# Kernel optimization log

Measured on AMD Instinct MI355X. Metric: run time of the kernel, lower is better.

Reference implementation:

```python
import jax, jax.numpy as jnp
import numpy as np

B, TMAX, C, H, NCLS = 256, 512, 128, 256, 400


def _lengths():
    rs = np.random.RandomState(0)
    lens = rs.randint(128, TMAX + 1, size=B)
    lens[0] = TMAX  # pin max length so T = TMAX
    return lens


def setup_inputs() -> dict:
    lens = _lengths()
    total = int(lens.sum())
    key = jax.random.key(0)
    ks = jax.random.split(key, 12)
    s_in, s_h = 1.0 / np.sqrt(C), 1.0 / np.sqrt(H)
    return {
        "input_features": jax.random.normal(ks[0], (total, C), jnp.float32),
        "segment_lengths": jnp.asarray(lens, jnp.int32),
        "W_ih": jax.random.normal(ks[1], (4 * H, C), jnp.float32) * s_h,
        "W_hh": jax.random.normal(ks[2], (4 * H, H), jnp.float32) * s_h,
        "b_ih": jax.random.normal(ks[3], (4 * H,), jnp.float32) * s_h,
        "b_hh": jax.random.normal(ks[4], (4 * H,), jnp.float32) * s_h,
        "h0_W1": jax.random.normal(ks[5], (C, C), jnp.float32) * s_in,
        "h0_W2": jax.random.normal(ks[6], (H, C), jnp.float32) * s_in,
        "c0_W1": jax.random.normal(ks[7], (C, C), jnp.float32) * s_in,
        "c0_W2": jax.random.normal(ks[8], (H, C), jnp.float32) * s_in,
        "fc_W": jax.random.normal(ks[9], (NCLS, H), jnp.float32) * s_h,
        "fc_b": jax.random.normal(ks[10], (NCLS,), jnp.float32) * s_h,
    }


def _lstm_step(x, h, c, W_ih, W_hh, b_ih, b_hh):
    # torch.nn.LSTMCell gate order: i, f, g, o
    gates = x @ W_ih.T + b_ih + h @ W_hh.T + b_hh
    i, f, g, o = jnp.split(gates, 4, axis=-1)
    c_new = jax.nn.sigmoid(f) * c + jax.nn.sigmoid(i) * jnp.tanh(g)
    h_new = jax.nn.sigmoid(o) * jnp.tanh(c_new)
    return h_new, c_new


def reference(input_features, segment_lengths, W_ih, W_hh, b_ih, b_hh,
              h0_W1, h0_W2, c0_W1, c0_W2, fc_W, fc_b):
    lens = np.asarray(segment_lengths)            # static ragged structure
    nb = lens.shape[0]
    T = int(lens.max())
    seg_id = np.repeat(np.arange(nb), lens)       # [total]
    offs = np.concatenate([np.arange(l) for l in lens])
    dt = input_features.dtype

    # pad_sequence(batch_first=True): [B, T, C]
    padded = jnp.zeros((nb, T, input_features.shape[1]), dt)
    padded = padded.at[jnp.asarray(seg_id), jnp.asarray(offs)].set(input_features)

    # 'input_means' in the original is actually a per-segment SUM
    sums = jax.ops.segment_sum(input_features, jnp.asarray(seg_id), num_segments=nb)
    h0 = jax.nn.relu(sums @ h0_W1.T) @ h0_W2.T
    c0 = jax.nn.relu(sums @ c0_W1.T) @ c0_W2.T

    def step(carry, x_t):
        h, c = carry
        h, c = _lstm_step(x_t, h, c, W_ih, W_hh, b_ih, b_hh)
        return (h, c), h

    xs = jnp.transpose(padded, (1, 0, 2))         # [T, B, C]
    _, h_outs = jax.lax.scan(step, (h0, c0), xs)  # [T, B, H]

    # Faithful to the original: h_outs is stacked time-first, yet indexed
    # h_outs[i, :segment_len] with i = batch index -> for segment i, mean over
    # the first min(len_i, B) BATCH rows of the hidden state at time t=i.
    lens_j = jnp.asarray(lens)
    mask = (jnp.arange(nb)[None, :] < lens_j[:, None]).astype(dt)   # [B(i), B(b)]
    count = jnp.minimum(lens_j, nb).astype(dt)                       # slice clamps at B
    fc_in = jnp.einsum('ib,ibh->ih', mask, h_outs[:nb]) / count[:, None]

    return fc_in @ fc_W.T + fc_b
```

## Files before the change

### kernel.cpp

```cpp
#include <hip/hip_runtime.h>
#include <hip/hip_bf16.h>
#include <stdint.h>

#define NB    256
#define CIN   128
#define HID   256
#define TST   256
#define NCLS  400

#define GRPS  16
#define MEMB  4
#define BPG   16
#define HPB   64
#define RPB   256
#define HXS   392
#define SPP   17

#define WS_SUMS   0u
#define WS_HEX0   131072u
#define WS_HEX    262144u
#define WS_C0     524288u
#define WS_PP     786432u

typedef __attribute__((ext_vector_type(8))) short bf16x8;
typedef __attribute__((ext_vector_type(4))) float f32x4;
typedef unsigned long long u64;

__device__ __forceinline__ short f2bf(float f) {
  __hip_bfloat16 h = __float2bfloat16(f);
  return *reinterpret_cast<short*>(&h);
}
__device__ __forceinline__ float sigm(float v) { return 1.0f / (1.0f + __expf(-v)); }
__device__ __forceinline__ float tanh_(float v) {
  v = fminf(fmaxf(v, -15.0f), 15.0f);
  const float e = __expf(2.0f * v);
  return (e - 1.0f) / (e + 1.0f);
}
__device__ __forceinline__ int q12(float h) {
  int q = (int)rintf(h * 2048.f);
  q = max(-2048, min(2047, q));
  return q & 0xFFF;
}
__device__ __forceinline__ short dq12(int bits) {
  int q = (bits ^ 0x800) - 0x800;
  return f2bf((float)q * (1.0f / 2048.f));
}

__global__ void k_segsum(const float* __restrict__ x, const int* __restrict__ lens,
                         float* __restrict__ sums) {
  const int b = blockIdx.x, t = threadIdx.x;
  __shared__ int   s_l[NB];
  __shared__ int   s_red[256];
  __shared__ float s_f[CIN];
  s_l[t] = lens[t];
  __syncthreads();
  int part = 0;
  for (int i = t; i < b; i += 256) part += s_l[i];
  s_red[t] = part; __syncthreads();
  for (int k = 128; k > 0; k >>= 1) { if (t < k) s_red[t] += s_red[t + k]; __syncthreads(); }
  const int off = s_red[0];
  const int len = s_l[b];
  const int c = t & 127, half = t >> 7;
  float a = 0.f;
  for (int r = half; r < len; r += 2) a += x[(size_t)(off + r) * CIN + c];
  if (half) s_f[c] = a;
  __syncthreads();
  if (!half) sums[b * CIN + c] = a + s_f[c];
}

__global__ void k_init(const float* __restrict__ sums,
                       const float* __restrict__ w1h, const float* __restrict__ w2h,
                       const float* __restrict__ w1c, const float* __restrict__ w2c,
                       u64* __restrict__ hex0, float* __restrict__ c0) {
  const int b = blockIdx.x, t = threadIdx.x;
  __shared__ float s_in[CIN], s_h[CIN], s_c[CIN];
  __shared__ __align__(8) short s_hb[HID];
  if (t < CIN) s_in[t] = sums[b * CIN + t];
  __syncthreads();
  {
    const int j = t & 127;
    const float* w = (t < CIN ? w1h : w1c) + j * CIN;
    float a = 0.f;
    #pragma unroll 8
    for (int k = 0; k < CIN; k++) a += s_in[k] * w[k];
    a = fmaxf(a, 0.f);
    if (t < CIN) s_h[j] = a; else s_c[j] = a;
  }
  __syncthreads();
  float ah = 0.f, ac = 0.f;
  const float* wh = w2h + t * CIN;
  const float* wc = w2c + t * CIN;
  #pragma unroll 8
  for (int k = 0; k < CIN; k++) { ah += s_h[k] * wh[k]; ac += s_c[k] * wc[k]; }
  s_hb[t] = f2bf(ah);
  c0[b * HID + t] = ac;
  __syncthreads();
  if (t < HID / 4)
    hex0[(size_t)b * 64 + t] = *(const u64*)&s_hb[t * 4];
}

__launch_bounds__(1024, 1)
__global__ void k_lstm(const float* __restrict__ x, const int* __restrict__ lens,
                       const float* __restrict__ Wih, const float* __restrict__ Whh,
                       const float* __restrict__ bih, const float* __restrict__ bhh,
                       const float* __restrict__ c0,
                       const u64* __restrict__ hex0, u64* __restrict__ hexch,
                       float* __restrict__ pp) {
  const int p    = blockIdx.x;
  const int m    = p >> 4;
  const int grp  = p & 15;
  const int bat0 = grp * BPG;
  const int hid0 = m * HPB;

  const int t   = threadIdx.x;
  const int w   = t >> 6;
  const int kq  = w & 3;
  const int mq  = w >> 2;
  const int l15 = t & 15;
  const int hi  = (t >> 4) & 3;

  const int j2 = t & 63, b2 = t >> 6;
  const int ch = t & 127, bp2 = (t >> 7) * 2;

  __shared__ __align__(16) short s_hxb[BPG * HXS];
  __shared__ float s_part[4 * RPB * SPP];
  __shared__ float s_red[1024];
  __shared__ __align__(8) short s_hvalb[1024];
  __shared__ int   s_lens[NB];
  __shared__ int   s_off[BPG], s_len[BPG];

  if (t < NB) s_lens[t] = lens[t];
  __syncthreads();
  if (t < BPG) {
    int off = 0;
    for (int k = 0; k < bat0 + t; k++) off += s_lens[k];
    s_off[t] = off;
    s_len[t] = s_lens[bat0 + t];
  }
  __syncthreads();

  #define LOADA(AV, MT, KC) do {                                                   \
    const int lr_   = (MT) * 16 + l15;                                             \
    const int grow_ = (lr_ >> 6) * HID + hid0 + (lr_ & 63);                        \
    const int k0_   = kq * 96 + (KC) * 32 + hi * 8;                                \
    const float* src_ = (k0_ < CIN) ? (Wih + (size_t)grow_ * CIN + k0_)            \
                                    : (Whh + (size_t)grow_ * HID + (k0_ - CIN));   \
    const float4 f0_ = *(const float4*)(src_);                                     \
    const float4 f1_ = *(const float4*)(src_ + 4);                                 \
    AV[0]=f2bf(f0_.x); AV[1]=f2bf(f0_.y); AV[2]=f2bf(f0_.z); AV[3]=f2bf(f0_.w);    \
    AV[4]=f2bf(f1_.x); AV[5]=f2bf(f1_.y); AV[6]=f2bf(f1_.z); AV[7]=f2bf(f1_.w);    \
  } while (0)
  bf16x8 a00, a01, a02, a10, a11, a12, a20, a21, a22, a30, a31, a32;
  LOADA(a00, mq*4+0, 0); LOADA(a01, mq*4+0, 1); LOADA(a02, mq*4+0, 2);
  LOADA(a10, mq*4+1, 0); LOADA(a11, mq*4+1, 1); LOADA(a12, mq*4+1, 2);
  LOADA(a20, mq*4+2, 0); LOADA(a21, mq*4+2, 1); LOADA(a22, mq*4+2, 2);
  LOADA(a30, mq*4+3, 0); LOADA(a31, mq*4+3, 1); LOADA(a32, mq*4+3, 2);

  const float bias0 = bih[0*HID + hid0 + j2] + bhh[0*HID + hid0 + j2];
  const float bias1 = bih[1*HID + hid0 + j2] + bhh[1*HID + hid0 + j2];
  const float bias2 = bih[2*HID + hid0 + j2] + bhh[2*HID + hid0 + j2];
  const float bias3 = bih[3*HID + hid0 + j2] + bhh[3*HID + hid0 + j2];

  float c_reg = c0[(size_t)(bat0 + b2) * HID + hid0 + j2];

  float xp0, xp1;
  #define PREFX(S) do { \
    xp0 = ((S) < s_len[bp2+0]) ? x[(size_t)(s_off[bp2+0]+(S))*CIN+ch] : 0.f; \
    xp1 = ((S) < s_len[bp2+1]) ? x[(size_t)(s_off[bp2+1]+(S))*CIN+ch] : 0.f; \
  } while (0)

  #define STAGE0() do { \
    s_hxb[(bp2+0)*HXS+ch] = f2bf(xp0); \
    s_hxb[(bp2+1)*HXS+ch] = f2bf(xp1); \
    const int b_ = t >> 6, q64_ = t & 63; \
    const u64 v_ = hex0[(size_t)(bat0 + b_) * 64 + q64_]; \
    *(u64*)&s_hxb[b_ * HXS + CIN + q64_ * 4] = v_; \
  } while (0)

  #define STAGE(S) do { \
    s_hxb[(bp2+0)*HXS+ch] = f2bf(xp0); \
    s_hxb[(bp2+1)*HXS+ch] = f2bf(xp1); \
    const int b_ = t >> 6, q64_ = t & 63; \
    const int mem_ = q64_ >> 4; \
    if (mem_ == m) { \
      *(u64*)&s_hxb[b_ * HXS + CIN + q64_ * 4] = \
          *(const u64*)&s_hvalb[b_ * HPB + (q64_ & 15) * 4]; \
    } else { \
      const u64* src_ = hexch + ((size_t)((S) & 1) * NB + bat0 + b_) * 64 + q64_; \
      u64 v_ = __hip_atomic_load(src_, __ATOMIC_RELAXED, __HIP_MEMORY_SCOPE_AGENT); \
      while ((v_ >> 48) != (u64)(S)) { \
        __builtin_amdgcn_s_sleep(1); \
        v_ = __hip_atomic_load(src_, __ATOMIC_RELAXED, __HIP_MEMORY_SCOPE_AGENT); \
      } \
      short* dst_ = &s_hxb[b_ * HXS + CIN + q64_ * 4]; \
      dst_[0] = dq12((int)(v_        & 0xFFF)); \
      dst_[1] = dq12((int)((v_ >> 12) & 0xFFF)); \
      dst_[2] = dq12((int)((v_ >> 24) & 0xFFF)); \
      dst_[3] = dq12((int)((v_ >> 36) & 0xFFF)); \
    } \
  } while (0)

  PREFX(0);
  STAGE0();
  __syncthreads();

  for (int s = 0; s < TST; s++) {
    f32x4 d0 = {0.f,0.f,0.f,0.f}, d1 = {0.f,0.f,0.f,0.f};
    f32x4 d2 = {0.f,0.f,0.f,0.f}, d3 = {0.f,0.f,0.f,0.f};
    {
      const short* hxb = s_hxb + l15 * HXS + kq * 96 + hi * 8;
      bf16x8 bv;
      bv = *(const bf16x8*)(hxb + 0);
      d0 = __builtin_amdgcn_mfma_f32_16x16x32_bf16(a00, bv, d0, 0, 0, 0);
      d1 = __builtin_amdgcn_mfma_f32_16x16x32_bf16(a10, bv, d1, 0, 0, 0);
      d2 = __builtin_amdgcn_mfma_f32_16x16x32_bf16(a20, bv, d2, 0, 0, 0);
      d3 = __builtin_amdgcn_mfma_f32_16x16x32_bf16(a30, bv, d3, 0, 0, 0);
      bv = *(const bf16x8*)(hxb + 32);
      d0 = __builtin_amdgcn_mfma_f32_16x16x32_bf16(a01, bv, d0, 0, 0, 0);
      d1 = __builtin_amdgcn_mfma_f32_16x16x32_bf16(a11, bv, d1, 0, 0, 0);
      d2 = __builtin_amdgcn_mfma_f32_16x16x32_bf16(a21, bv, d2, 0, 0, 0);
      d3 = __builtin_amdgcn_mfma_f32_16x16x32_bf16(a31, bv, d3, 0, 0, 0);
      bv = *(const bf16x8*)(hxb + 64);
      d0 = __builtin_amdgcn_mfma_f32_16x16x32_bf16(a02, bv, d0, 0, 0, 0);
      d1 = __builtin_amdgcn_mfma_f32_16x16x32_bf16(a12, bv, d1, 0, 0, 0);
      d2 = __builtin_amdgcn_mfma_f32_16x16x32_bf16(a22, bv, d2, 0, 0, 0);
      d3 = __builtin_amdgcn_mfma_f32_16x16x32_bf16(a32, bv, d3, 0, 0, 0);
    }
    if (s < TST - 1) PREFX(s + 1);

    {
      float* spc = s_part + (size_t)(kq * RPB + mq * 64 + hi * 4) * SPP + l15;
      spc[(0*16 + 0)*SPP] = d0[0]; spc[(0*16 + 1)*SPP] = d0[1];
      spc[(0*16 + 2)*SPP] = d0[2]; spc[(0*16 + 3)*SPP] = d0[3];
      spc[(1*16 + 0)*SPP] = d1[0]; spc[(1*16 + 1)*SPP] = d1[1];
      spc[(1*16 + 2)*SPP] = d1[2]; spc[(1*16 + 3)*SPP] = d1[3];
      spc[(2*16 + 0)*SPP] = d2[0]; spc[(2*16 + 1)*SPP] = d2[1];
      spc[(2*16 + 2)*SPP] = d2[2]; spc[(2*16 + 3)*SPP] = d2[3];
      spc[(3*16 + 0)*SPP] = d3[0]; spc[(3*16 + 1)*SPP] = d3[1];
      spc[(3*16 + 2)*SPP] = d3[2]; spc[(3*16 + 3)*SPP] = d3[3];
    }
    __syncthreads();

    float g0 = bias0, g1 = bias1, g2 = bias2, g3 = bias3;
    #pragma unroll
    for (int q = 0; q < 4; q++) {
      const float* spq = s_part + (size_t)(q * RPB + j2) * SPP + b2;
      g0 += spq[(0 * 64) * SPP];
      g1 += spq[(1 * 64) * SPP];
      g2 += spq[(2 * 64) * SPP];
      g3 += spq[(3 * 64) * SPP];
    }
    c_reg = fmaf(sigm(g1), c_reg, sigm(g0) * tanh_(g2));
    const float h = sigm(g3) * tanh_(c_reg);

    {
      const int q  = q12(h);
      const int qp = q | (__shfl_xor(q, 1) << 12);
      const int qo = __shfl_xor(qp, 2);
      if ((t & 3) == 0) {
        const u64 v = ((u64)(s + 1) << 48) |
                      ((u64)(unsigned)(qo & 0xFFFFFF) << 24) |
                      (u64)(unsigned)(qp & 0xFFFFFF);
        __hip_atomic_store(
            hexch + ((size_t)((s + 1) & 1) * NB + bat0 + b2) * 64 + (hid0 >> 2) + (j2 >> 2),
            v, __ATOMIC_RELAXED, __HIP_MEMORY_SCOPE_AGENT);
      }
    }
    s_hvalb[b2 * HPB + j2] = f2bf(h);
    s_red[b2 * HPB + j2]   = (bat0 + b2 < s_lens[s]) ? h : 0.f;
    __syncthreads();

    if (t >= 512 && t < 512 + HPB) {
      const int jl = t - 512;
      float ps = 0.f;
      #pragma unroll
      for (int b = 0; b < BPG; b++) ps += s_red[b * HPB + jl];
      pp[(((size_t)s * GRPS + grp) * MEMB + m) * HPB + jl] = ps;
    }

    if (s == TST - 1) break;

    STAGE(s + 1);
    __syncthreads();
  }
}

__global__ void k_out(const float* __restrict__ pp, const int* __restrict__ lens,
                      const float* __restrict__ fcW, const float* __restrict__ fcb,
                      float* __restrict__ out) {
  const int i = blockIdx.x, t = threadIdx.x;
  __shared__ float s_fc[HID];
  const int cnt = min(lens[i], NB);
  const int m = t >> 6, jl = t & 63;
  float a = 0.f;
  const float* base = pp + ((size_t)i * GRPS * MEMB + m) * HPB + jl;
  #pragma unroll 4
  for (int g = 0; g < GRPS; g++) a += base[(size_t)g * MEMB * HPB];
  s_fc[t] = a / (float)cnt;
  __syncthreads();
  for (int n = t; n < NCLS; n += 256) {
    float acc = fcb[n];
    const float4* w4 = (const float4*)(fcW + (size_t)n * HID);
    #pragma unroll 8
    for (int k4 = 0; k4 < HID / 4; k4++) {
      const float4 wv = w4[k4];
      acc = fmaf(s_fc[4*k4+0], wv.x, acc);
      acc = fmaf(s_fc[4*k4+1], wv.y, acc);
      acc = fmaf(s_fc[4*k4+2], wv.z, acc);
      acc = fmaf(s_fc[4*k4+3], wv.w, acc);
    }
    out[(size_t)i * NCLS + n] = acc;
  }
}

extern "C" void kernel_launch(void* const* d_in, const int* in_sizes, int n_in,
                              void* d_out, int out_size, void* d_ws, size_t ws_size,
                              hipStream_t stream) {
  const float* x    = (const float*)d_in[0];
  const int*   lens = (const int*)  d_in[1];
  const float* Wih  = (const float*)d_in[2];
  const float* Whh  = (const float*)d_in[3];
  const float* bih  = (const float*)d_in[4];
  const float* bhh  = (const float*)d_in[5];
  const float* w1h  = (const float*)d_in[6];
  const float* w2h  = (const float*)d_in[7];
  const float* w1c  = (const float*)d_in[8];
  const float* w2c  = (const float*)d_in[9];
  const float* fcW  = (const float*)d_in[10];
  const float* fcb  = (const float*)d_in[11];
  float* out = (float*)d_out;

  char* ws = (char*)d_ws;
  float* sums = (float*)(ws + WS_SUMS);
  u64*   hex0 = (u64*)  (ws + WS_HEX0);
  u64*   hex  = (u64*)  (ws + WS_HEX);
  float* c0   = (float*)(ws + WS_C0);
  float* pp   = (float*)(ws + WS_PP);

  hipMemsetAsync(hex, 0, 2 * NB * 64 * sizeof(u64), stream);
  k_segsum<<<NB, 256, 0, stream>>>(x, lens, sums);
  k_init  <<<NB, 256, 0, stream>>>(sums, w1h, w2h, w1c, w2c, hex0, c0);
  k_lstm  <<<GRPS * MEMB, 1024, 0, stream>>>(x, lens, Wih, Whh, bih, bhh, c0, hex0, hex, pp);
  k_out   <<<NB, 256, 0, stream>>>(pp, lens, fcW, fcb, out);
}
```

Measured before the change: 836.2 us.

## Add fast sc0 hidden-state exchange path with agent-scope fallback and entry barrier

Each hidden-state packet is now written twice: once with sc0 loads/stores into a fast buffer and once with agent-scope atomics into a safe buffer. Readers spin briefly on the fast buffer, which is cheaper if the sharing blocks sit on the same XCD L2, and fall back to sleeping on the atomic buffer. The fast buffer is cleared inside the kernel, and a per-group entry barrier makes blocks wait until all members have finished that clear. The cost is extra stores every step and reliance on cache-coherence behaviour that is not guaranteed across XCDs.

```diff
diff --git a/kernel.cpp b/kernel.cpp
--- a/kernel.cpp
+++ b/kernel.cpp
@@ -18,9 +18,11 @@
 
 #define WS_SUMS   0u
 #define WS_HEX0   131072u
-#define WS_HEX    262144u
-#define WS_C0     524288u
-#define WS_PP     786432u
+#define WS_HEXS   262144u
+#define WS_ENT    524288u
+#define WS_HEXF   528384u
+#define WS_C0     790528u
+#define WS_PP     1052672u
 
 typedef __attribute__((ext_vector_type(8))) short bf16x8;
 typedef __attribute__((ext_vector_type(4))) float f32x4;
@@ -44,6 +46,16 @@
 __device__ __forceinline__ short dq12(int bits) {
   int q = (bits ^ 0x800) - 0x800;
   return f2bf((float)q * (1.0f / 2048.f));
+}
+
+__device__ __forceinline__ void st_sc0(u64* p, u64 v) {
+  asm volatile("global_store_dwordx2 %0, %1, off sc0" :: "v"(p), "v"(v) : "memory");
+}
+__device__ __forceinline__ u64 ld_sc0(const u64* p) {
+  u64 v;
+  asm volatile("global_load_dwordx2 %0, %1, off sc0\n\ts_waitcnt vmcnt(0)"
+               : "=v"(v) : "v"(p));
+  return v;
 }
 
 __global__ void k_segsum(const float* __restrict__ x, const int* __restrict__ lens,
@@ -104,8 +116,9 @@
                        const float* __restrict__ Wih, const float* __restrict__ Whh,
                        const float* __restrict__ bih, const float* __restrict__ bhh,
                        const float* __restrict__ c0,
-                       const u64* __restrict__ hex0, u64* __restrict__ hexch,
-                       float* __restrict__ pp) {
+                       const u64* __restrict__ hex0,
+                       u64* __restrict__ hexF, u64* __restrict__ hexS,
+                       float* __restrict__ pp, int* __restrict__ ent) {
   const int p    = blockIdx.x;
   const int m    = p >> 4;
   const int grp  = p & 15;
@@ -138,6 +151,13 @@
     s_len[t] = s_lens[bat0 + t];
   }
   __syncthreads();
+
+  #pragma unroll
+  for (int z = 0; z < 2; z++) {
+    const int idx = z * 1024 + t;
+    const int sl = idx >> 10, bb = (idx >> 6) & 15, qq = idx & 63;
+    st_sc0(hexF + ((size_t)(sl * NB) + bat0 + bb) * 64 + qq, 0ULL);
+  }
 
   #define LOADA(AV, MT, KC) do {                                                   \
     const int lr_   = (MT) * 16 + l15;                                             \
@@ -163,6 +183,15 @@
 
   float c_reg = c0[(size_t)(bat0 + b2) * HID + hid0 + j2];
 
+  asm volatile("s_waitcnt vmcnt(0)" ::: "memory");
+  __syncthreads();
+  if (t == 0) {
+    __hip_atomic_fetch_add(ent + grp * 16, 1, __ATOMIC_RELAXED, __HIP_MEMORY_SCOPE_AGENT);
+    while (__hip_atomic_load(ent + grp * 16, __ATOMIC_RELAXED, __HIP_MEMORY_SCOPE_AGENT) < MEMB)
+      __builtin_amdgcn_s_sleep(1);
+  }
+  __syncthreads();
+
   float xp0, xp1;
   #define PREFX(S) do { \
     xp0 = ((S) < s_len[bp2+0]) ? x[(size_t)(s_off[bp2+0]+(S))*CIN+ch] : 0.f; \
@@ -186,11 +215,14 @@
       *(u64*)&s_hxb[b_ * HXS + CIN + q64_ * 4] = \
           *(const u64*)&s_hvalb[b_ * HPB + (q64_ & 15) * 4]; \
     } else { \
-      const u64* src_ = hexch + ((size_t)((S) & 1) * NB + bat0 + b_) * 64 + q64_; \
-      u64 v_ = __hip_atomic_load(src_, __ATOMIC_RELAXED, __HIP_MEMORY_SCOPE_AGENT); \
-      while ((v_ >> 48) != (u64)(S)) { \
-        __builtin_amdgcn_s_sleep(1); \
-        v_ = __hip_atomic_load(src_, __ATOMIC_RELAXED, __HIP_MEMORY_SCOPE_AGENT); \
+      const size_t off_ = ((size_t)((((S) & 1)) * NB) + bat0 + b_) * 64 + q64_; \
+      u64 v_ = ld_sc0(hexF + off_); \
+      int tries_ = 0; \
+      while ((v_ >> 48) != (u64)(S) && ++tries_ < 32) v_ = ld_sc0(hexF + off_); \
+      if ((v_ >> 48) != (u64)(S)) { \
+        do { __builtin_amdgcn_s_sleep(1); \
+             v_ = __hip_atomic_load(hexS + off_, __ATOMIC_RELAXED, __HIP_MEMORY_SCOPE_AGENT); \
+        } while ((v_ >> 48) != (u64)(S)); \
       } \
       short* dst_ = &s_hxb[b_ * HXS + CIN + q64_ * 4]; \
       dst_[0] = dq12((int)(v_        & 0xFFF)); \
@@ -261,9 +293,10 @@
         const u64 v = ((u64)(s + 1) << 48) |
                       ((u64)(unsigned)(qo & 0xFFFFFF) << 24) |
                       (u64)(unsigned)(qp & 0xFFFFFF);
-        __hip_atomic_store(
-            hexch + ((size_t)((s + 1) & 1) * NB + bat0 + b2) * 64 + (hid0 >> 2) + (j2 >> 2),
-            v, __ATOMIC_RELAXED, __HIP_MEMORY_SCOPE_AGENT);
+        const size_t off = ((size_t)(((s + 1) & 1) * NB) + bat0 + b2) * 64 +
+                           (hid0 >> 2) + (j2 >> 2);
+        st_sc0(hexF + off, v);
+        __hip_atomic_store(hexS + off, v, __ATOMIC_RELAXED, __HIP_MEMORY_SCOPE_AGENT);
       }
     }
     s_hvalb[b2 * HPB + j2] = f2bf(h);
@@ -333,13 +366,16 @@
   char* ws = (char*)d_ws;
   float* sums = (float*)(ws + WS_SUMS);
   u64*   hex0 = (u64*)  (ws + WS_HEX0);
-  u64*   hex  = (u64*)  (ws + WS_HEX);
+  u64*   hexS = (u64*)  (ws + WS_HEXS);
+  int*   ent  = (int*)  (ws + WS_ENT);
+  u64*   hexF = (u64*)  (ws + WS_HEXF);
   float* c0   = (float*)(ws + WS_C0);
   float* pp   = (float*)(ws + WS_PP);
 
-  hipMemsetAsync(hex, 0, 2 * NB * 64 * sizeof(u64), stream);
+  hipMemsetAsync(hexS, 0, 2 * NB * 64 * sizeof(u64) + 1024, stream);
   k_segsum<<<NB, 256, 0, stream>>>(x, lens, sums);
   k_init  <<<NB, 256, 0, stream>>>(sums, w1h, w2h, w1c, w2c, hex0, c0);
-  k_lstm  <<<GRPS * MEMB, 1024, 0, stream>>>(x, lens, Wih, Whh, bih, bhh, c0, hex0, hex, pp);
+  k_lstm  <<<GRPS * MEMB, 1024, 0, stream>>>(x, lens, Wih, Whh, bih, bhh, c0,
+                                             hex0, hexF, hexS, pp, ent);
   k_out   <<<NB, 256, 0, stream>>>(pp, lens, fcW, fcb, out);
 }
```

Result: slower. 1.807 ms (+116.1%).
